# Kernel optimization log

Hardware: AMD Instinct MI355X
Metric: run time of the kernel (lower is better)

Reference implementation:

```python
import jax, jax.numpy as jnp
import numpy as np

N = 100000      # nodes
F_IN = 512      # num_features
H = 256         # hidden
C = 64          # num_classes
E = 3200000     # edges
K = 10          # APPNP propagation steps
ALPHA = 0.1     # teleport probability


def setup_inputs() -> dict:
    key = jax.random.key(0)
    k_x, k_w0, k_w1, k_e = jax.random.split(key, 4)
    x = jax.random.normal(k_x, (N, F_IN), dtype=jnp.float32)
    w0 = jax.random.normal(k_w0, (F_IN, H), dtype=jnp.float32) / np.sqrt(F_IN).astype(np.float32)
    b0 = jnp.zeros((H,), dtype=jnp.float32)
    w1 = jax.random.normal(k_w1, (H, C), dtype=jnp.float32) / np.sqrt(H).astype(np.float32)
    b1 = jnpps = jnp.zeros((C,), dtype=jnp.float32)
    edge_index = jax.random.randint(k_e, (2, E), 0, N, dtype=jnp.int64)
    return {"x": x, "w0": w0, "b0": b0, "w1": w1, "b1": b1, "edge_index": edge_index}


def _appnp(h, edge_index):
    # Add self loops (PyG APPNP default: gcn_norm with self loops).
    loops = jnp.arange(N, dtype=edge_index.dtype)
    src = jnp.concatenate([edge_index[0], loops])
    dst = jnp.concatenate([edge_index[1], loops])
    # Symmetric GCN normalization: D^{-1/2} (A+I) D^{-1/2}
    deg = jax.ops.segment_sum(jnp.ones_like(src, dtype=h.dtype), dst, num_segments=N)
    dinv = jnp.where(deg > 0, jax.lax.rsqrt(deg), 0.0)
    norm = dinv[src] * dinv[dst]  # [E+N]

    def step(xc, _):
        msg = norm[:, None] * xc[src]                      # gather [E+N, C]
        agg = jax.ops.segment_sum(msg, dst, num_segments=N)  # scatter-add [N, C]
        return (1.0 - ALPHA) * agg + ALPHA * h, None

    out, _ = jax.lax.scan(step, h, None, length=K)
    return out


def reference(x, w0, b0, w1, b1, edge_index):
    # eval mode: dropout is identity
    h = jax.nn.relu(x @ w0 + b0)   # [N, H]
    h = h @ w1 + b1                # [N, C]
    z = _appnp(h, edge_index)      # [N, C]
    return jax.nn.log_softmax(z, axis=1)
```

## Files before the change

### kernel.cpp

```cpp
#include <hip/hip_runtime.h>
#include <hip/hip_bf16.h>

#define NN 100000
#define EE 3200000
#define FIN 512
#define HH 256
#define CC 64
#define KSTEPS 10
#define SB 391
#define NBUC 782
#define EPB 4096
#define NEB 782
#define NB_X2B 2048
#define NB_PREP 576

typedef __attribute__((ext_vector_type(8))) short bf16x8;
typedef __attribute__((ext_vector_type(8))) short s16x8;
typedef __attribute__((ext_vector_type(4))) float f32x4;
typedef unsigned short ushort_t;

__device__ __forceinline__ short f2bf(float f) {
    union { __hip_bfloat16 h; short s; } u;
    u.h = __float2bfloat16(f);
    return u.s;
}

__device__ __forceinline__ void glds16(const void* g, void* l) {
    __builtin_amdgcn_global_load_lds(
        (const __attribute__((address_space(1))) void*)g,
        (__attribute__((address_space(3))) void*)l, 16, 0, 0);
}


__device__ void dev_x2b(int bx, const float* __restrict__ x, ushort_t* __restrict__ xb) {
    const long NTOT = (long)NN * FIN;
    const long stride = (long)NB_X2B * 256 * 8;
    for (long i = ((long)bx * 256 + threadIdx.x) * 8; i < NTOT; i += stride) {
        float4 a = *(const float4*)(x + i);
        float4 b = *(const float4*)(x + i + 4);
        s16x8 o;
        o[0] = f2bf(a.x); o[1] = f2bf(a.y); o[2] = f2bf(a.z); o[3] = f2bf(a.w);
        o[4] = f2bf(b.x); o[5] = f2bf(b.y); o[6] = f2bf(b.z); o[7] = f2bf(b.w);
        *(s16x8*)(xb + i) = o;
    }
}

__device__ void dev_prep_w(int bx, const float* __restrict__ w0, const float* __restrict__ w1,
                           short* __restrict__ w0t, short* __restrict__ w1t) {
    int t = bx * 256 + threadIdx.x;
    if (t < FIN * HH) {
        int k = t >> 8, n = t & 255;
        w0t[n * FIN + k] = f2bf(w0[t]);
    } else if (t < FIN * HH + HH * CC) {
        int u = t - FIN * HH;
        int k = u >> 6, n = u & 63;
        w1t[n * HH + k] = f2bf(w1[u]);
    }
}

__device__ void dev_bincnt(int bx, const int* __restrict__ ei, int* __restrict__ bcnt,
                           int* __restrict__ hb) {
    int tid = threadIdx.x;
    int base = bx * EPB;
    for (int i = tid; i < NBUC; i += 256) hb[i] = 0;
    __syncthreads();
#pragma unroll 4
    for (int i = 0; i < EPB / 256; ++i) {
        int t = base + i * 256 + tid;
        if (t < EE) atomicAdd(&hb[(unsigned)ei[EE + t] >> 7], 1);
    }
    __syncthreads();
    for (int i = tid; i < NBUC; i += 256)
        if (hb[i]) atomicAdd(&bcnt[i], hb[i]);
}

__global__ __launch_bounds__(256) void fused1(const float* __restrict__ x,
                                              ushort_t* __restrict__ xb,
                                              const int* __restrict__ ei,
                                              int* __restrict__ bcnt,
                                              const float* __restrict__ w0,
                                              const float* __restrict__ w1,
                                              short* __restrict__ w0t,
                                              short* __restrict__ w1t) {
    __shared__ int hb[NBUC];
    int bx = blockIdx.x;
    if (bx < NB_X2B) dev_x2b(bx, x, xb);
    else if (bx < NB_X2B + NEB) dev_bincnt(bx - NB_X2B, ei, bcnt, hb);
    else dev_prep_w(bx - NB_X2B - NEB, w0, w1, w0t, w1t);
}


__global__ __launch_bounds__(1024) void bscan(const int* __restrict__ bcnt,
                                              int* __restrict__ eboff) {
    __shared__ int sh[1024];
    int t = threadIdx.x;
    int v = (t < NBUC) ? bcnt[t] : 0;
    sh[t] = v;
    __syncthreads();
    for (int off = 1; off < 1024; off <<= 1) {
        int add = (t >= off) ? sh[t - off] : 0;
        __syncthreads();
        sh[t] += add;
        __syncthreads();
    }
    if (t < NBUC) eboff[t] = sh[t] - v;
}

__global__ __launch_bounds__(256) void binfill(const int* __restrict__ ei,
                                               const int* __restrict__ eboff,
                                               int* __restrict__ bfc,
                                               int* __restrict__ stg) {
    __shared__ int hb[NBUC];
    __shared__ int lb[NBUC];
    int tid = threadIdx.x;
    int base = blockIdx.x * EPB;
    for (int i = tid; i < NBUC; i += 256) hb[i] = 0;
    __syncthreads();
#pragma unroll 4
    for (int i = 0; i < EPB / 256; ++i) {
        int t = base + i * 256 + tid;
        if (t < EE) atomicAdd(&hb[(unsigned)ei[EE + t] >> 7], 1);
    }
    __syncthreads();
    for (int i = tid; i < NBUC; i += 256) {
        int c = hb[i];
        lb[i] = eboff[i] + (c ? atomicAdd(&bfc[i], c) : 0);
        hb[i] = 0;
    }
    __syncthreads();
#pragma unroll 4
    for (int i = 0; i < EPB / 256; ++i) {
        int t = base + i * 256 + tid;
        if (t < EE) {
            int s = ei[t];
            int d = ei[EE + t];
            int b = (unsigned)d >> 7;
            int o = atomicAdd(&hb[b], 1);
            stg[lb[b] + o] = (s << 7) | (d & 127);
        }
    }
}

__global__ __launch_bounds__(256) void bucket_finish(
    const int* __restrict__ stg, const int* __restrict__ eboff,
    const int* __restrict__ bcnt,
    int* __restrict__ cnt, float* __restrict__ dinv, float* __restrict__ wco,
    float* __restrict__ sdg, int* __restrict__ rp, int* __restrict__ eds,
    int* __restrict__ dbc) {
    __shared__ int nc8[128 * 8];
    __shared__ int nc[128];
    __shared__ int sc[128];
    __shared__ int lrp[128];
    __shared__ int h64[64];
    int b = blockIdx.x, tid = threadIdx.x;
    int nodes = min(128, NN - b * 128);
    for (int i = tid; i < 128 * 8; i += 256) nc8[i] = 0;
    if (tid < 64) h64[tid] = 0;
    __syncthreads();
    int s0 = eboff[b], n = bcnt[b];
    for (int i = tid; i < n; i += 256) {
        int e = stg[s0 + i];
        atomicAdd(&nc8[(e & 127) * 8 + ((e >> 7) >> 14)], 1);
    }
    __syncthreads();
    if (tid < 128) {
        int excl = 0;
#pragma unroll
        for (int r = 0; r < 8; ++r) {
            int c = nc8[tid * 8 + r];
            nc8[tid * 8 + r] = excl;
            excl += c;
        }
        nc[tid] = excl;
        sc[tid] = (tid < nodes) ? excl + 1 : 0;
    }
    __syncthreads();
    for (int off = 1; off < 128; off <<= 1) {
        int add = (tid < 128 && tid >= off) ? sc[tid - off] : 0;
        __syncthreads();
        if (tid < 128) sc[tid] += add;
        __syncthreads();
    }
    int base = eboff[b] + b * 128;
    if (tid < nodes) {
        int node = b * 128 + tid;
        int c = nc[tid];
        int excl = base + sc[tid] - (c + 1);
        lrp[tid] = excl;
        rp[node] = excl;
        cnt[node] = c;
        float fd = (float)(c + 1);
        dinv[node] = rsqrtf(fd);
        wco[node] = 0.9f / fd;
        sdg[node] = sqrtf(fd);
        atomicAdd(&h64[min(c, 63)], 1);
    }
    if (b == NBUC - 1 && tid == 0) rp[NN] = base + n + nodes;
    __syncthreads();
    if (tid < 64 && h64[tid]) atomicAdd(&dbc[tid], h64[tid]);
    for (int i = tid; i < n; i += 256) {
        int e = stg[s0 + i];
        int src = e >> 7, loc = e & 127;
        int o = atomicAdd(&nc8[loc * 8 + (src >> 14)], 1);
        eds[lrp[loc] + o] = src;
    }
    __syncthreads();
    if (tid < nodes) eds[lrp[tid] + nc[tid]] = b * 128 + tid;
}

__global__ void dscan(const int* __restrict__ dbc, int* __restrict__ dboff) {
    __shared__ int sh[64];
    int t = threadIdx.x;
    int v = dbc[t];
    sh[t] = v;
    __syncthreads();
    for (int off = 1; off < 64; off <<= 1) {
        int add = (t >= off) ? sh[t - off] : 0;
        __syncthreads();
        sh[t] += add;
        __syncthreads();
    }
    dboff[t] = sh[t] - v;
}

__global__ __launch_bounds__(256) void dperm(const int* __restrict__ cnt,
                                             const int* __restrict__ dboff,
                                             int* __restrict__ dfc,
                                             int* __restrict__ perm) {
    __shared__ int h[64];
    __shared__ int base[64];
    int tid = threadIdx.x;
    int i = blockIdx.x * 256 + tid;
    if (tid < 64) h[tid] = 0;
    __syncthreads();
    int bin = 0, r = 0;
    bool ok = i < NN;
    if (ok) {
        bin = min(cnt[i], 63);
        r = atomicAdd(&h[bin], 1);
    }
    __syncthreads();
    if (tid < 64) {
        int c = h[tid];
        base[tid] = dboff[tid] + (c ? atomicAdd(&dfc[tid], c) : 0);
    }
    __syncthreads();
    if (ok) perm[base[bin] + r] = i;
}

__global__ __launch_bounds__(256) void gemm1(const ushort_t* __restrict__ xb,
                                             const short* __restrict__ w0t,
                                             const float* __restrict__ b0,
                                             short* __restrict__ h0) {
    __shared__ __align__(16) short As[2][128 * 64];
    __shared__ __align__(16) short Bs[2][128 * 64];
    const int tid = threadIdx.x;
    const int lane = tid & 63;
    const int wid = tid >> 6;
    const int wm = wid >> 1, wn = wid & 1;
    const int bn0 = blockIdx.x * 128;
    const long row0 = (long)blockIdx.y * 128;
    const int rl = lane >> 3;
    const int gko = (lane & 7) ^ rl;

    auto stage = [&](int kt, int buf) {
#pragma unroll
        for (int j = 0; j < 4; ++j) {
            int blk = wid * 4 + j;
            const ushort_t* g = xb + (row0 + blk * 8 + rl) * FIN + kt * 64 + gko * 8;
            glds16(g, &As[buf][blk * 512]);
        }
#pragma unroll
        for (int j = 0; j < 4; ++j) {
            int blk = wid * 4 + j;
            const short* g = w0t + (size_t)(bn0 + blk * 8 + rl) * FIN + kt * 64 + gko * 8;
            glds16(g, &Bs[buf][blk * 512]);
        }
    };

    f32x4 acc[4][4] = {};
    stage(0, 0);
    __syncthreads();
    for (int kt = 0; kt < FIN / 64; ++kt) {
        int cur = kt & 1;
        if (kt < FIN / 64 - 1) stage(kt + 1, cur ^ 1);
#pragma unroll
        for (int ks = 0; ks < 2; ++ks) {
            int ko = ks * 4 + (lane >> 4);
            int slot = ko ^ (lane & 7);
            bf16x8 af[4], bfr[4];
#pragma unroll
            for (int i = 0; i < 4; ++i) {
                int row = wm * 64 + i * 16 + (lane & 15);
                af[i] = *(const bf16x8*)(&As[cur][(row * 8 + slot) * 8]);
            }
#pragma unroll
            for (int j = 0; j < 4; ++j) {
                int col = wn * 64 + j * 16 + (lane & 15);
                bfr[j] = *(const bf16x8*)(&Bs[cur][(col * 8 + slot) * 8]);
            }
#pragma unroll
            for (int i = 0; i < 4; ++i)
#pragma unroll
                for (int j = 0; j < 4; ++j)
                    acc[i][j] = __builtin_amdgcn_mfma_f32_16x16x32_bf16(af[i], bfr[j], acc[i][j], 0, 0, 0);
        }
        __syncthreads();
    }
#pragma unroll
    for (int j = 0; j < 4; ++j) {
        int gcol = bn0 + wn * 64 + j * 16 + (lane & 15);
        float bias = b0[gcol];
#pragma unroll
        for (int i = 0; i < 4; ++i)
#pragma unroll
            for (int q = 0; q < 4; ++q) {
                long grow = row0 + wm * 64 + i * 16 + (lane >> 4) * 4 + q;
                float v = acc[i][j][q] + bias;
                if (v < 0.f) v = 0.f;
                h0[grow * HH + gcol] = f2bf(v);
            }
    }
}

__global__ __launch_bounds__(256) void gemm2(const short* __restrict__ h0,
                                             const short* __restrict__ w1t,
                                             const float* __restrict__ b1,
                                             const float* __restrict__ dinv,
                                             ushort_t* __restrict__ hvb,
                                             ushort_t* __restrict__ v0) {
    __shared__ __align__(16) short As[2][128 * 64];
    __shared__ __align__(16) short Bs[2][64 * 64];
    const int tid = threadIdx.x;
    const int lane = tid & 63;
    const int wid = tid >> 6;
    const int wm = wid >> 1, wn = wid & 1;
    const long row0 = (long)blockIdx.x * 128;
    const int rl = lane >> 3;
    const int gko = (lane & 7) ^ rl;

    auto stage = [&](int kt, int buf) {
#pragma unroll
        for (int j = 0; j < 4; ++j) {
            int blk = wid * 4 + j;
            const short* g = h0 + (row0 + blk * 8 + rl) * HH + kt * 64 + gko * 8;
            glds16(g, &As[buf][blk * 512]);
        }
#pragma unroll
        for (int j = 0; j < 2; ++j) {
            int blk = wid * 2 + j;
            const short* g = w1t + (size_t)(blk * 8 + rl) * HH + kt * 64 + gko * 8;
            glds16(g, &Bs[buf][blk * 512]);
        }
    };

    f32x4 acc[4][2] = {};
    stage(0, 0);
    __syncthreads();
    for (int kt = 0; kt < HH / 64; ++kt) {
        int cur = kt & 1;
        if (kt < HH / 64 - 1) stage(kt + 1, cur ^ 1);
#pragma unroll
        for (int ks = 0; ks < 2; ++ks) {
            int ko = ks * 4 + (lane >> 4);
            int slot = ko ^ (lane & 7);
            bf16x8 af[4], bfr[2];
#pragma unroll
            for (int i = 0; i < 4; ++i) {
                int row = wm * 64 + i * 16 + (lane & 15);
                af[i] = *(const bf16x8*)(&As[cur][(row * 8 + slot) * 8]);
            }
#pragma unroll
            for (int j = 0; j < 2; ++j) {
                int col = wn * 32 + j * 16 + (lane & 15);
                bfr[j] = *(const bf16x8*)(&Bs[cur][(col * 8 + slot) * 8]);
            }
#pragma unroll
            for (int i = 0; i < 4; ++i)
#pragma unroll
                for (int j = 0; j < 2; ++j)
                    acc[i][j] = __builtin_amdgcn_mfma_f32_16x16x32_bf16(af[i], bfr[j], acc[i][j], 0, 0, 0);
        }
        __syncthreads();
    }
#pragma unroll
    for (int i = 0; i < 4; ++i)
#pragma unroll
        for (int j = 0; j < 2; ++j) {
            int col = wn * 32 + j * 16 + (lane & 15);
            float bias = b1[col];
#pragma unroll
            for (int q = 0; q < 4; ++q) {
                long grow = row0 + wm * 64 + i * 16 + (lane >> 4) * 4 + q;
                if (grow < NN) {
                    float hval = acc[i][j][q] + bias;
                    float dv = dinv[grow];
                    hvb[grow * CC + col] = (ushort_t)f2bf(0.1f * dv * hval);
                    v0[grow * CC + col] = (ushort_t)f2bf(dv * hval);
                }
            }
        }
}

__device__ __forceinline__ void gath(float a[8], const ushort_t* __restrict__ vin,
                                     int src, int l) {
    const int4 r = *(const int4*)(vin + ((size_t)src << 6) + (l << 3));
    a[0] += __int_as_float(r.x << 16);
    a[1] += __int_as_float(r.x & 0xffff0000);
    a[2] += __int_as_float(r.y << 16);
    a[3] += __int_as_float(r.y & 0xffff0000);
    a[4] += __int_as_float(r.z << 16);
    a[5] += __int_as_float(r.z & 0xffff0000);
    a[6] += __int_as_float(r.w << 16);
    a[7] += __int_as_float(r.w & 0xffff0000);
}

template <int LAST>
__global__ __launch_bounds__(256) void prop(const ushort_t* __restrict__ vin,
                                            const ushort_t* __restrict__ hvb,
                                            const float* __restrict__ wco,
                                            const float* __restrict__ sdg,
                                            ushort_t* __restrict__ vout,
                                            float* __restrict__ zout,
                                            const int* __restrict__ rp,
                                            const int* __restrict__ eds,
                                            const int* __restrict__ perm) {
    int g = perm[blockIdx.x * 32 + (threadIdx.x >> 3)];
    int l = threadIdx.x & 7;
    int beg = rp[g], end = rp[g + 1];
    float a0[8] = {}, a1[8] = {}, a2[8] = {}, a3[8] = {};
    int e = beg;
    int head = (beg + 3) & ~3;
    if (head > end) head = end;
    for (; e < head; ++e) gath(a0, vin, eds[e], l);
    for (; e + 3 < end; e += 4) {
        int4 ee = *(const int4*)(eds + e);
        gath(a0, vin, ee.x, l);
        gath(a1, vin, ee.y, l);
        gath(a2, vin, ee.z, l);
        gath(a3, vin, ee.w, l);
    }
    for (; e < end; ++e) gath(a1, vin, eds[e], l);

    float w = wco[g];
    const int4 hb = *(const int4*)(hvb + ((size_t)g << 6) + (l << 3));
    float tv[8];
    tv[0] = __int_as_float(hb.x << 16);
    tv[1] = __int_as_float(hb.x & 0xffff0000);
    tv[2] = __int_as_float(hb.y << 16);
    tv[3] = __int_as_float(hb.y & 0xffff0000);
    tv[4] = __int_as_float(hb.z << 16);
    tv[5] = __int_as_float(hb.z & 0xffff0000);
    tv[6] = __int_as_float(hb.w << 16);
    tv[7] = __int_as_float(hb.w & 0xffff0000);
    float r[8];
#pragma unroll
    for (int c = 0; c < 8; ++c)
        r[c] = w * ((a0[c] + a1[c]) + (a2[c] + a3[c])) + tv[c];
    if (!LAST) {
        s16x8 o;
#pragma unroll
        for (int c = 0; c < 8; ++c) o[c] = f2bf(r[c]);
        *(s16x8*)(vout + ((size_t)g << 6) + (l << 3)) = o;
    } else {
        float sd = sdg[g];
#pragma unroll
        for (int c = 0; c < 8; ++c) r[c] *= sd;
        float m = r[0];
#pragma unroll
        for (int c = 1; c < 8; ++c) m = fmaxf(m, r[c]);
#pragma unroll
        for (int off = 1; off < 8; off <<= 1) m = fmaxf(m, __shfl_xor(m, off));
        float s = 0.f;
#pragma unroll
        for (int c = 0; c < 8; ++c) s += expf(r[c] - m);
#pragma unroll
        for (int off = 1; off < 8; off <<= 1) s += __shfl_xor(s, off);
        float ls = m + logf(s);
        f32x4 o0, o1;
#pragma unroll
        for (int c = 0; c < 4; ++c) { o0[c] = r[c] - ls; o1[c] = r[c + 4] - ls; }
        *(f32x4*)(zout + ((size_t)g << 6) + (l << 3)) = o0;
        *(f32x4*)(zout + ((size_t)g << 6) + (l << 3) + 4) = o1;
    }
}

extern "C" void kernel_launch(void* const* d_in, const int* in_sizes, int n_in,
                              void* d_out, int out_size, void* d_ws, size_t ws_size,
                              hipStream_t stream) {
    const float* x  = (const float*)d_in[0];
    const float* w0 = (const float*)d_in[1];
    const float* b0 = (const float*)d_in[2];
    const float* w1 = (const float*)d_in[3];
    const float* b1 = (const float*)d_in[4];
    const int*   ei = (const int*)d_in[5];

    char* ws = (char*)d_ws;
    size_t off = 0;
    auto take = [&](size_t n) { size_t r = off; off += (n + 255) & ~(size_t)255; return r; };
    size_t o_h0    = take((size_t)100096 * HH * 2);
    size_t o_vA    = take((size_t)NN * CC * 2);
    size_t o_hv    = take((size_t)NN * CC * 2);
    size_t o_ed    = take((size_t)(EE + NN) * 4);
    size_t o_rp    = take((size_t)(NN + 1) * 4);
    size_t o_cnt   = take((size_t)NN * 4);
    size_t o_dinv  = take((size_t)NN * 4);
    size_t o_wco   = take((size_t)NN * 4);
    size_t o_sdg   = take((size_t)NN * 4);
    size_t o_perm  = take((size_t)NN * 4);
    size_t o_w0t   = take((size_t)HH * FIN * 2);
    size_t o_w1t   = take((size_t)CC * HH * 2);
    size_t o_eboff = take((size_t)NBUC * 4);
    size_t o_dboff = take((size_t)64 * 4);
    size_t o_z     = take((size_t)(NBUC + NBUC + 64 + 64) * 4);
    size_t o_xb    = take((size_t)100096 * FIN * 2);

    short*    h0    = (short*)(ws + o_h0);
    ushort_t* vA    = (ushort_t*)(ws + o_vA);
    ushort_t* vB    = (ushort_t*)(ws + o_h0);
    ushort_t* hvb   = (ushort_t*)(ws + o_hv);
    int*      stg   = (int*)(ws + o_hv);
    int*      eds   = (int*)(ws + o_ed);
    int*      rp    = (int*)(ws + o_rp);
    int*      cnt   = (int*)(ws + o_cnt);
    float*    dinv  = (float*)(ws + o_dinv);
    float*    wco   = (float*)(ws + o_wco);
    float*    sdg   = (float*)(ws + o_sdg);
    int*      perm  = (int*)(ws + o_perm);
    short*    w0t   = (short*)(ws + o_w0t);
    short*    w1t   = (short*)(ws + o_w1t);
    int*      eboff = (int*)(ws + o_eboff);
    int*      dboff = (int*)(ws + o_dboff);
    int*      bcnt  = (int*)(ws + o_z);
    int*      bfc   = bcnt + NBUC;
    int*      dbc   = bfc + NBUC;
    int*      dfc   = dbc + 64;
    ushort_t* xb    = (ushort_t*)(ws + o_xb);
    float*    zout  = (float*)d_out;

    hipMemsetAsync(ws + o_z, 0, (size_t)(NBUC + NBUC + 64 + 64) * 4, stream);

    fused1<<<NB_X2B + NEB + NB_PREP, 256, 0, stream>>>(x, xb, ei, bcnt, w0, w1, w0t, w1t);
    bscan<<<1, 1024, 0, stream>>>(bcnt, eboff);
    binfill<<<NEB, 256, 0, stream>>>(ei, eboff, bfc, stg);
    bucket_finish<<<NBUC, 256, 0, stream>>>(stg, eboff, bcnt, cnt, dinv, wco, sdg, rp, eds, dbc);
    dscan<<<1, 64, 0, stream>>>(dbc, dboff);
    dperm<<<SB, 256, 0, stream>>>(cnt, dboff, dfc, perm);

    gemm1<<<dim3(2, 782), 256, 0, stream>>>(xb, w0t, b0, h0);
    gemm2<<<782, 256, 0, stream>>>(h0, w1t, b1, dinv, hvb, vA);

    const ushort_t* in = vA;
    for (int k = 0; k < KSTEPS; ++k) {
        if (k == KSTEPS - 1) {
            prop<1><<<NN / 32, 256, 0, stream>>>(in, hvb, wco, sdg, nullptr, zout, rp, eds, perm);
        } else {
            ushort_t* o = (k & 1) ? vA : vB;
            prop<0><<<NN / 32, 256, 0, stream>>>(in, hvb, wco, sdg, o, nullptr, rp, eds, perm);
            in = o;
        }
    }
}
```

Baseline: 860.5 us.

## Merge edge bin-fill and first GEMM into one interleaved launch

Folds the edge bucket-fill kernel and the first dense GEMM into a single launch. Blocks are interleaved so that every third block does bin-fill and the others do GEMM tiles, sharing one 64KB shared-memory pool. This lets the atomic-heavy scatter pass overlap with the compute-bound GEMM and removes one launch boundary. The cost is that bin-fill blocks now reserve 64KB of LDS, which may lower their occupancy.

```diff
diff --git a/kernel.cpp b/kernel.cpp
--- a/kernel.cpp
+++ b/kernel.cpp
@@ -106,14 +106,12 @@
     if (t < NBUC) eboff[t] = sh[t] - v;
 }
 
-__global__ __launch_bounds__(256) void binfill(const int* __restrict__ ei,
-                                               const int* __restrict__ eboff,
-                                               int* __restrict__ bfc,
-                                               int* __restrict__ stg) {
-    __shared__ int hb[NBUC];
-    __shared__ int lb[NBUC];
+__device__ void dev_binfill(int bx, const int* __restrict__ ei, const int* __restrict__ eboff,
+                            int* __restrict__ bfc, int* __restrict__ stg, int* pool) {
+    int* hb = pool;
+    int* lb = pool + NBUC;
     int tid = threadIdx.x;
-    int base = blockIdx.x * EPB;
+    int base = bx * EPB;
     for (int i = tid; i < NBUC; i += 256) hb[i] = 0;
     __syncthreads();
 #pragma unroll 4
@@ -139,6 +137,94 @@
             stg[lb[b] + o] = (s << 7) | (d & 127);
         }
     }
+}
+
+__device__ void dev_gemm1(int g1, const ushort_t* __restrict__ xb,
+                          const short* __restrict__ w0t, const float* __restrict__ b0,
+                          short* __restrict__ h0, char* sm) {
+    short* AsP = (short*)sm;
+    short* BsP = (short*)(sm + 32768);
+    const int tid = threadIdx.x;
+    const int lane = tid & 63;
+    const int wid = tid >> 6;
+    const int wm = wid >> 1, wn = wid & 1;
+    const int bn0 = (g1 & 1) * 128;
+    const long row0 = (long)(g1 >> 1) * 128;
+    const int rl = lane >> 3;
+    const int gko = (lane & 7) ^ rl;
+
+    auto stage = [&](int kt, int buf) {
+#pragma unroll
+        for (int j = 0; j < 4; ++j) {
+            int blk = wid * 4 + j;
+            const ushort_t* g = xb + (row0 + blk * 8 + rl) * FIN + kt * 64 + gko * 8;
+            glds16(g, &AsP[buf * 8192 + blk * 512]);
+        }
+#pragma unroll
+        for (int j = 0; j < 4; ++j) {
+            int blk = wid * 4 + j;
+            const short* g = w0t + (size_t)(bn0 + blk * 8 + rl) * FIN + kt * 64 + gko * 8;
+            glds16(g, &BsP[buf * 8192 + blk * 512]);
+        }
+    };
+
+    f32x4 acc[4][4] = {};
+    stage(0, 0);
+    __syncthreads();
+    for (int kt = 0; kt < FIN / 64; ++kt) {
+        int cur = kt & 1;
+        if (kt < FIN / 64 - 1) stage(kt + 1, cur ^ 1);
+#pragma unroll
+        for (int ks = 0; ks < 2; ++ks) {
+            int ko = ks * 4 + (lane >> 4);
+            int slot = ko ^ (lane & 7);
+            bf16x8 af[4], bfr[4];
+#pragma unroll
+            for (int i = 0; i < 4; ++i) {
+                int row = wm * 64 + i * 16 + (lane & 15);
+                af[i] = *(const bf16x8*)(&AsP[cur * 8192 + (row * 8 + slot) * 8]);
+            }
+#pragma unroll
+            for (int j = 0; j < 4; ++j) {
+                int col = wn * 64 + j * 16 + (lane & 15);
+                bfr[j] = *(const bf16x8*)(&BsP[cur * 8192 + (col * 8 + slot) * 8]);
+            }
+#pragma unroll
+            for (int i = 0; i < 4; ++i)
+#pragma unroll
+                for (int j = 0; j < 4; ++j)
+                    acc[i][j] = __builtin_amdgcn_mfma_f32_16x16x32_bf16(af[i], bfr[j], acc[i][j], 0, 0, 0);
+        }
+        __syncthreads();
+    }
+#pragma unroll
+    for (int j = 0; j < 4; ++j) {
+        int gcol = bn0 + wn * 64 + j * 16 + (lane & 15);
+        float bias = b0[gcol];
+#pragma unroll
+        for (int i = 0; i < 4; ++i)
+#pragma unroll
+            for (int q = 0; q < 4; ++q) {
+                long grow = row0 + wm * 64 + i * 16 + (lane >> 4) * 4 + q;
+                float v = acc[i][j][q] + bias;
+                if (v < 0.f) v = 0.f;
+                h0[grow * HH + gcol] = f2bf(v);
+            }
+    }
+}
+
+__global__ __launch_bounds__(256) void fused3(const int* __restrict__ ei,
+                                              const int* __restrict__ eboff,
+                                              int* __restrict__ bfc,
+                                              int* __restrict__ stg,
+                                              const ushort_t* __restrict__ xb,
+                                              const short* __restrict__ w0t,
+                                              const float* __restrict__ b0,
+                                              short* __restrict__ h0) {
+    __shared__ __align__(16) char sm[65536];
+    int bx = blockIdx.x, r = bx % 3, q = bx / 3;
+    if (r == 2) dev_binfill(q, ei, eboff, bfc, stg, (int*)sm);
+    else dev_gemm1(q * 2 + r, xb, w0t, b0, h0, sm);
 }
 
 __global__ __launch_bounds__(256) void bucket_finish(
@@ -246,81 +332,6 @@
     }
     __syncthreads();
     if (ok) perm[base[bin] + r] = i;
-}
-
-__global__ __launch_bounds__(256) void gemm1(const ushort_t* __restrict__ xb,
-                                             const short* __restrict__ w0t,
-                                             const float* __restrict__ b0,
-                                             short* __restrict__ h0) {
-    __shared__ __align__(16) short As[2][128 * 64];
-    __shared__ __align__(16) short Bs[2][128 * 64];
-    const int tid = threadIdx.x;
-    const int lane = tid & 63;
-    const int wid = tid >> 6;
-    const int wm = wid >> 1, wn = wid & 1;
-    const int bn0 = blockIdx.x * 128;
-    const long row0 = (long)blockIdx.y * 128;
-    const int rl = lane >> 3;
-    const int gko = (lane & 7) ^ rl;
-
-    auto stage = [&](int kt, int buf) {
-#pragma unroll
-        for (int j = 0; j < 4; ++j) {
-            int blk = wid * 4 + j;
-            const ushort_t* g = xb + (row0 + blk * 8 + rl) * FIN + kt * 64 + gko * 8;
-            glds16(g, &As[buf][blk * 512]);
-        }
-#pragma unroll
-        for (int j = 0; j < 4; ++j) {
-            int blk = wid * 4 + j;
-            const short* g = w0t + (size_t)(bn0 + blk * 8 + rl) * FIN + kt * 64 + gko * 8;
-            glds16(g, &Bs[buf][blk * 512]);
-        }
-    };
-
-    f32x4 acc[4][4] = {};
-    stage(0, 0);
-    __syncthreads();
-    for (int kt = 0; kt < FIN / 64; ++kt) {
-        int cur = kt & 1;
-        if (kt < FIN / 64 - 1) stage(kt + 1, cur ^ 1);
-#pragma unroll
-        for (int ks = 0; ks < 2; ++ks) {
-            int ko = ks * 4 + (lane >> 4);
-            int slot = ko ^ (lane & 7);
-            bf16x8 af[4], bfr[4];
-#pragma unroll
-            for (int i = 0; i < 4; ++i) {
-                int row = wm * 64 + i * 16 + (lane & 15);
-                af[i] = *(const bf16x8*)(&As[cur][(row * 8 + slot) * 8]);
-            }
-#pragma unroll
-            for (int j = 0; j < 4; ++j) {
-                int col = wn * 64 + j * 16 + (lane & 15);
-                bfr[j] = *(const bf16x8*)(&Bs[cur][(col * 8 + slot) * 8]);
-            }
-#pragma unroll
-            for (int i = 0; i < 4; ++i)
-#pragma unroll
-                for (int j = 0; j < 4; ++j)
-                    acc[i][j] = __builtin_amdgcn_mfma_f32_16x16x32_bf16(af[i], bfr[j], acc[i][j], 0, 0, 0);
-        }
-        __syncthreads();
-    }
-#pragma unroll
-    for (int j = 0; j < 4; ++j) {
-        int gcol = bn0 + wn * 64 + j * 16 + (lane & 15);
-        float bias = b0[gcol];
-#pragma unroll
-        for (int i = 0; i < 4; ++i)
-#pragma unroll
-            for (int q = 0; q < 4; ++q) {
-                long grow = row0 + wm * 64 + i * 16 + (lane >> 4) * 4 + q;
-                float v = acc[i][j][q] + bias;
-                if (v < 0.f) v = 0.f;
-                h0[grow * HH + gcol] = f2bf(v);
-            }
-    }
 }
 
 __global__ __launch_bounds__(256) void gemm2(const short* __restrict__ h0,
@@ -542,12 +553,11 @@
 
     fused1<<<NB_X2B + NEB + NB_PREP, 256, 0, stream>>>(x, xb, ei, bcnt, w0, w1, w0t, w1t);
     bscan<<<1, 1024, 0, stream>>>(bcnt, eboff);
-    binfill<<<NEB, 256, 0, stream>>>(ei, eboff, bfc, stg);
+    fused3<<<NBUC * 3, 256, 0, stream>>>(ei, eboff, bfc, stg, xb, w0t, b0, h0);
     bucket_finish<<<NBUC, 256, 0, stream>>>(stg, eboff, bcnt, cnt, dinv, wco, sdg, rp, eds, dbc);
     dscan<<<1, 64, 0, stream>>>(dbc, dboff);
     dperm<<<SB, 256, 0, stream>>>(cnt, dboff, dfc, perm);
 
-    gemm1<<<dim3(2, 782), 256, 0, stream>>>(xb, w0t, b0, h0);
     gemm2<<<782, 256, 0, stream>>>(h0, w1t, b1, dinv, hvb, vA);
 
     const ushort_t* in = vA;
```

Measured after the change: 819.9 us. -4.7%, faster.
